# Performance work log

Hardware: AMD Instinct MI355X
Metric: run time of the kernel (lower is better)

Reference implementation:

```python
import jax, jax.numpy as jnp
import jax.scipy as jsp
import numpy as np

NUM_EMBEDDINGS = 256
EMBEDDING_DIM = 64
SPARSITY_LEVEL = 4
N_BINS = 16
COEF_MAX = 3.0
COEF_MU = 50.0
COMMITMENT_COST = 0.25
EPSILON = 1e-10


def _normalize_dict(dictionary):
    # F.normalize(dict, p=2, dim=0, eps): x / max(||x||_2, eps) per column
    nrm = jnp.linalg.norm(dictionary, axis=0, keepdims=True)
    return dictionary / jnp.maximum(nrm, EPSILON)


def _quantize_coeff_mu_law(coeff):
    inv_log1p_mu = 1.0 / np.log1p(COEF_MU)  # scalar constant
    c = jnp.clip(coeff, -COEF_MAX, COEF_MAX) / COEF_MAX
    encoded = jnp.sign(c) * jnp.log1p(jnp.abs(c) * COEF_MU) * inv_log1p_mu
    scaled = (encoded + 1.0) * ((N_BINS - 1) / 2.0)
    bin_idx = jnp.clip(jnp.round(scaled).astype(jnp.int32), 0, N_BINS - 1)
    # dequantize
    z = bin_idx.astype(coeff.dtype) * (2.0 / (N_BINS - 1)) - 1.0
    decoded = jnp.sign(z) * (jnp.expm1(jnp.abs(z) / inv_log1p_mu) / COEF_MU) * COEF_MAX
    return bin_idx, decoded


def batch_omp_with_support(X, Dn, K):
    # X: [M, Bs] signals, Dn: [M, N] normalized dictionary
    G = Dn.T @ Dn                       # [N, N] Gram
    h_bar = (Dn.T @ X).T                # [Bs, N] correlations
    Bs, N = h_bar.shape
    dt = h_bar.dtype
    h = h_bar
    mask = jnp.zeros((Bs, N), dtype=bool)
    L = jnp.ones((Bs, 1, 1), dtype=dt)  # incremental Cholesky of G[I, I]
    I = jnp.zeros((Bs, 0), dtype=jnp.int32)
    x_sel = jnp.zeros((Bs, 0), dtype=dt)
    rows = jnp.arange(Bs)
    for k in range(1, K + 1):  # K is small & static -> unrolled
        idx = jnp.argmax(jnp.abs(h) * (~mask), axis=1).astype(jnp.int32)
        mask = mask.at[rows, idx].set(True)
        if k > 1:
            G_stack = G[I, idx[:, None]]                     # [Bs, k-1]
            w = jsp.linalg.solve_triangular(L, G_stack[..., None], lower=True)  # [Bs,k-1,1]
            wT = jnp.swapaxes(w, 1, 2)                       # [Bs,1,k-1]
            w_corner = jnp.sqrt(jnp.clip(1.0 - jnp.sum(wT * wT, axis=2, keepdims=True), 1e-12))
            top = jnp.concatenate([L, jnp.zeros((Bs, k - 1, 1), dt)], axis=2)
            bot = jnp.concatenate([wT, w_corner], axis=2)
            L = jnp.concatenate([top, bot], axis=1)          # [Bs,k,k]
        I = jnp.concatenate([I, idx[:, None]], axis=1)       # [Bs,k]
        h_stack = jnp.take_along_axis(h_bar, I, axis=1)[..., None]  # [Bs,k,1]
        # cholesky_solve: L L^T x = h
        y = jsp.linalg.solve_triangular(L, h_stack, lower=True)
        xs = jsp.linalg.solve_triangular(jnp.swapaxes(L, 1, 2), y, lower=False)
        x_sel = xs[..., 0]                                   # [Bs,k] coeffs aligned w/ support
        beta = jnp.einsum('bk,bkn->bn', x_sel, G[I])         # [Bs,N]
        h = h_bar - beta
    return I, x_sel


def setup_inputs() -> dict:
    key = jax.random.key(0)
    k1, k2 = jax.random.split(key)
    z_e = jax.random.normal(k1, (32, EMBEDDING_DIM, 64, 64), dtype=jnp.float32)
    dictionary = jax.random.normal(k2, (EMBEDDING_DIM, NUM_EMBEDDINGS), dtype=jnp.float32) * 0.02
    return {"z_e": z_e, "dictionary": dictionary}


def reference(z_e, dictionary):
    B, C, H, W = z_e.shape
    Dn = _normalize_dict(dictionary)
    signals = jnp.transpose(z_e, (0, 2, 3, 1)).reshape(-1, C).T  # [C, B*H*W]
    # OMP runs with no grad (torch.no_grad in original)
    support, coeffs = jax.lax.stop_gradient(
        batch_omp_with_support(jax.lax.stop_gradient(signals), jax.lax.stop_gradient(Dn), SPARSITY_LEVEL)
    )
    # mu-law quantize coefficients (constants w.r.t. grads)
    bin_idx, coeffs_q = _quantize_coeff_mu_law(coeffs)
    # reconstruct with quantized coeffs; dictionary path is differentiable
    atoms = Dn.T[support]                                    # [Bs, K, C]
    recon_flat = jnp.einsum('bkc,bk->bc', atoms, coeffs_q)
    recon = jnp.transpose(recon_flat.reshape(B, H, W, C), (0, 3, 1, 2))
    # VQ-VAE style losses + STE
    e_latent_loss = jnp.mean((jax.lax.stop_gradient(recon) - z_e) ** 2)
    q_latent_loss = jnp.mean((recon - jax.lax.stop_gradient(z_e)) ** 2)
    loss = q_latent_loss + COMMITMENT_COST * e_latent_loss
    z_q = z_e + jax.lax.stop_gradient(recon - z_e)
    return z_q, loss


if __name__ == '__main__':
    out = reference(**setup_inputs())
    print(out[0].shape, out[1])
```

## Files before the change

### kernel.cpp

```cpp
#include <hip/hip_runtime.h>
#include <math.h>

#define NEMB 256
#define DIM 64
#define SIGS_B 64
#define THREADS 256
#define NSIG 131072
#define GRID (NSIG / SIGS_B)

#define LOG1P50 3.9318256327243257
#define INV_MU_F ((float)(1.0 / LOG1P50))
#define TWO15_F ((float)(2.0 / 15.0))

#define LB_SIG   0
#define LB_XS    16384
#define LB_QI    17408
#define LB_RED   18432
#define LDS_BYTES 18464

typedef float f2 __attribute__((ext_vector_type(2)));

__device__ __forceinline__ float rdlane_f(float v, int lane)
{
    return __builtin_bit_cast(float, __builtin_amdgcn_readlane(__builtin_bit_cast(int, v), lane));
}

template<int CTRL>
__device__ __forceinline__ float dpp_fmax(float m)
{
    int sh = __builtin_amdgcn_update_dpp(0, __builtin_bit_cast(int, m), CTRL, 0xf, 0xf, true);
    return fmaxf(m, __builtin_bit_cast(float, sh));
}

__device__ __forceinline__ float wave_max_nn(float v)
{
    v = dpp_fmax<0x111>(v);
    v = dpp_fmax<0x112>(v);
    v = dpp_fmax<0x114>(v);
    v = dpp_fmax<0x118>(v);
    v = dpp_fmax<0x142>(v);
    v = dpp_fmax<0x143>(v);
    return v;
}

__global__ void k_ng(const float* __restrict__ D, float* __restrict__ Dn,
                     float* __restrict__ DnT, float* __restrict__ G,
                     double* __restrict__ loss_acc, unsigned int* __restrict__ ctr)
{
#pragma clang fp contract(off)
    __shared__ float nrmS[NEMB];
    __shared__ float coli[DIM];
    int i = blockIdx.x, j = threadIdx.x;
    if (i == 0 && j == 0) { loss_acc[0] = 0.0; ctr[0] = 0u; }
    float ss = 0.0f;
    for (int c = 0; c < DIM; c++) {
        float v = D[c * NEMB + j];
        float sq = v * v;
        ss = ss + sq;
    }
    float nrm = fmaxf(sqrtf(ss), 1e-10f);
    nrmS[j] = nrm;
    __syncthreads();
    if (j < DIM) {
        float dni = D[j * NEMB + i] / nrmS[i];
        coli[j] = dni;
        Dn[j * NEMB + i] = dni;
        DnT[i * DIM + j] = dni;
    }
    __syncthreads();
    float s = 0.0f;
#pragma unroll 8
    for (int c = 0; c < DIM; c++) {
        float dnj = D[c * NEMB + j] / nrm;
        s = fmaf(coli[c], dnj, s);
    }
    G[i * NEMB + j] = s;
}

__device__ __forceinline__ float quant_decode(float coeff)
{
#pragma clang fp contract(off)
    float c = fminf(fmaxf(coeff, -3.0f), 3.0f) / 3.0f;
    float ac = fabsf(c);
    float sgn = (c > 0.0f) ? 1.0f : ((c < 0.0f) ? -1.0f : 0.0f);
    float l = log1pf(ac * 50.0f);
    float enc = (sgn * l) * INV_MU_F;
    float scaled = (enc + 1.0f) * 7.5f;
    int bin = (int)rintf(scaled);
    bin = bin < 0 ? 0 : (bin > 15 ? 15 : bin);
    float t = (float)bin * TWO15_F;
    float zv = t - 1.0f;
    float az = fabsf(zv);
    float sz = (zv > 0.0f) ? 1.0f : ((zv < 0.0f) ? -1.0f : 0.0f);
    float e = expm1f(az / INV_MU_F);
    return (sz * (e / 50.0f)) * 3.0f;
}

__device__ __forceinline__ void omp_quad(const f2 (*hbsi)[2], int lane, int qt,
                                         const float* __restrict__ G,
                                         float* __restrict__ xsv,
                                         int* __restrict__ qi, int s0)
{
#pragma clang fp contract(off)
    f2 h0[2] = {hbsi[0][0], hbsi[0][1]};
    f2 h1[2] = {hbsi[1][0], hbsi[1][1]};
    f2 h2[2] = {hbsi[2][0], hbsi[2][1]};
    f2 h3[2] = {hbsi[3][0], hbsi[3][1]};
    int m40 = 0, m41 = 0, m42 = 0, m43 = 0;
    int Iv0[4], Iv1[4], Iv2[4], Iv3[4];
    int Ivq[4];
    float L10, L11, L20, L21, L22, L30, L31, L32, L33;
    float y0, y1, y2, y3;
    float x0 = 0.f, x1 = 0.f, x2 = 0.f, x3 = 0.f;
#pragma unroll
    for (int kk = 0; kk < 4; kk++) {
        float bv0 = -1.f, bv1 = -1.f, bv2 = -1.f, bv3 = -1.f;
        int bj0 = 0, bj1 = 0, bj2 = 0, bj3 = 0;
#pragma unroll
        for (int j = 0; j < 4; j++) {
            float a0 = (m40 & (1 << j)) ? 0.f : fabsf(h0[j >> 1][j & 1]);
            if (a0 > bv0) { bv0 = a0; bj0 = j; }
            float a1 = (m41 & (1 << j)) ? 0.f : fabsf(h1[j >> 1][j & 1]);
            if (a1 > bv1) { bv1 = a1; bj1 = j; }
            float a2 = (m42 & (1 << j)) ? 0.f : fabsf(h2[j >> 1][j & 1]);
            if (a2 > bv2) { bv2 = a2; bj2 = j; }
            float a3 = (m43 & (1 << j)) ? 0.f : fabsf(h3[j >> 1][j & 1]);
            if (a3 > bv3) { bv3 = a3; bj3 = j; }
        }
        float r0 = wave_max_nn(bv0);
        float r1 = wave_max_nn(bv1);
        float r2 = wave_max_nn(bv2);
        float r3 = wave_max_nn(bv3);
        float vm0 = rdlane_f(r0, 63), vm1 = rdlane_f(r1, 63);
        float vm2 = rdlane_f(r2, 63), vm3 = rdlane_f(r3, 63);
        unsigned long long bl0 = __ballot(bv0 == vm0);
        unsigned long long bl1 = __ballot(bv1 == vm1);
        unsigned long long bl2 = __ballot(bv2 == vm2);
        unsigned long long bl3 = __ballot(bv3 == vm3);
        int ow0 = __ffsll((long long)bl0) - 1;
        int ow1 = __ffsll((long long)bl1) - 1;
        int ow2 = __ffsll((long long)bl2) - 1;
        int ow3 = __ffsll((long long)bl3) - 1;
        int bo0 = __builtin_amdgcn_readlane(bj0, ow0);
        int bo1 = __builtin_amdgcn_readlane(bj1, ow1);
        int bo2 = __builtin_amdgcn_readlane(bj2, ow2);
        int bo3 = __builtin_amdgcn_readlane(bj3, ow3);
        int id0 = 4 * ow0 + bo0;
        int id1 = 4 * ow1 + bo1;
        int id2 = 4 * ow2 + bo2;
        int id3 = 4 * ow3 + bo3;
        m40 |= (lane == ow0) ? (1 << bo0) : 0;
        m41 |= (lane == ow1) ? (1 << bo1) : 0;
        m42 |= (lane == ow2) ? (1 << bo2) : 0;
        m43 |= (lane == ow3) ? (1 << bo3) : 0;
        float tv0 = hbsi[0][0][0];
        tv0 = (bj0 == 1) ? hbsi[0][0][1] : tv0;
        tv0 = (bj0 == 2) ? hbsi[0][1][0] : tv0;
        tv0 = (bj0 == 3) ? hbsi[0][1][1] : tv0;
        float tv1 = hbsi[1][0][0];
        tv1 = (bj1 == 1) ? hbsi[1][0][1] : tv1;
        tv1 = (bj1 == 2) ? hbsi[1][1][0] : tv1;
        tv1 = (bj1 == 3) ? hbsi[1][1][1] : tv1;
        float tv2 = hbsi[2][0][0];
        tv2 = (bj2 == 1) ? hbsi[2][0][1] : tv2;
        tv2 = (bj2 == 2) ? hbsi[2][1][0] : tv2;
        tv2 = (bj2 == 3) ? hbsi[2][1][1] : tv2;
        float tv3 = hbsi[3][0][0];
        tv3 = (bj3 == 1) ? hbsi[3][0][1] : tv3;
        tv3 = (bj3 == 2) ? hbsi[3][1][0] : tv3;
        tv3 = (bj3 == 3) ? hbsi[3][1][1] : tv3;
        float hs0 = rdlane_f(tv0, ow0);
        float hs1 = rdlane_f(tv1, ow1);
        float hs2 = rdlane_f(tv2, ow2);
        float hs3 = rdlane_f(tv3, ow3);
        Iv0[kk] = id0; Iv1[kk] = id1; Iv2[kk] = id2; Iv3[kk] = id3;
        float hsel = (qt & 2) ? ((qt & 1) ? hs3 : hs2) : ((qt & 1) ? hs1 : hs0);
        int idxq = (qt & 2) ? ((qt & 1) ? id3 : id2) : ((qt & 1) ? id1 : id0);
        Ivq[kk] = idxq;
        float Gs0 = 0.f, Gs1 = 0.f, Gs2 = 0.f;
        if (kk > 0) Gs0 = G[(size_t)(Ivq[0] << 8) + idxq];
        if (kk > 1) Gs1 = G[(size_t)(Ivq[1] << 8) + idxq];
        if (kk > 2) Gs2 = G[(size_t)(Ivq[2] << 8) + idxq];
        if (kk == 1) {
            float cw0 = Gs0;
            float css = cw0 * cw0;
            float om = 1.0f - css;
            L10 = cw0;
            L11 = sqrtf(fmaxf(om, 1e-12f));
        }
        if (kk == 2) {
            float cw0 = Gs0;
            float ct = Gs1 - L10 * cw0;
            float cw1 = ct / L11;
            float css = cw0 * cw0;
            float cp = cw1 * cw1; css = css + cp;
            float om = 1.0f - css;
            L20 = cw0; L21 = cw1;
            L22 = sqrtf(fmaxf(om, 1e-12f));
        }
        if (kk == 3) {
            float cw0 = Gs0;
            float ct = Gs1 - L10 * cw0;
            float cw1 = ct / L11;
            float ca = L20 * cw0;
            float cp = L21 * cw1; ca = ca + cp;
            float ct3 = Gs2 - ca;
            float cw2 = ct3 / L22;
            float css = cw0 * cw0;
            cp = cw1 * cw1; css = css + cp;
            cp = cw2 * cw2; css = css + cp;
            float om = 1.0f - css;
            L30 = cw0; L31 = cw1; L32 = cw2;
            L33 = sqrtf(fmaxf(om, 1e-12f));
        }
        if (kk == 0) y0 = hsel;
        if (kk == 1) { float a = L10 * y0; y1 = (hsel - a) / L11; }
        if (kk == 2) { float a = L20 * y0; float p = L21 * y1; a = a + p;
                       y2 = (hsel - a) / L22; }
        if (kk == 3) { float a = L30 * y0; float p = L31 * y1; a = a + p;
                       p = L32 * y2; a = a + p;
                       y3 = (hsel - a) / L33; }
        if (kk == 0) { x0 = y0; }
        if (kk == 1) {
            x1 = y1 / L11;
            float a = L10 * x1;
            x0 = y0 - a;
        }
        if (kk == 2) {
            x2 = y2 / L22;
            float a = L21 * x2;
            x1 = (y1 - a) / L11;
            a = L10 * x1;
            float p = L20 * x2; a = a + p;
            x0 = y0 - a;
        }
        if (kk == 3) {
            x3 = y3 / L33;
            float a = L32 * x3;
            x2 = (y2 - a) / L22;
            a = L21 * x2;
            float p = L31 * x3; a = a + p;
            x1 = (y1 - a) / L11;
            a = L10 * x1;
            p = L20 * x2; a = a + p;
            p = L30 * x3; a = a + p;
            x0 = y0 - a;
        }
        if (kk < 3) {
            float xb00 = rdlane_f(x0, 0),  xb10 = rdlane_f(x0, 16);
            float xb20 = rdlane_f(x0, 32), xb30 = rdlane_f(x0, 48);
            float xb01 = 0.f, xb11 = 0.f, xb21 = 0.f, xb31 = 0.f;
            float xb02 = 0.f, xb12 = 0.f, xb22 = 0.f, xb32 = 0.f;
            if (kk > 0) { xb01 = rdlane_f(x1, 0);  xb11 = rdlane_f(x1, 16);
                          xb21 = rdlane_f(x1, 32); xb31 = rdlane_f(x1, 48); }
            if (kk > 1) { xb02 = rdlane_f(x2, 0);  xb12 = rdlane_f(x2, 16);
                          xb22 = rdlane_f(x2, 32); xb32 = rdlane_f(x2, 48); }
            const int l4 = 4 * lane;
            float4 R00 = *(const float4*)(G + ((size_t)Iv0[0] << 8) + l4);
            float4 R10 = *(const float4*)(G + ((size_t)Iv1[0] << 8) + l4);
            float4 R20 = *(const float4*)(G + ((size_t)Iv2[0] << 8) + l4);
            float4 R30 = *(const float4*)(G + ((size_t)Iv3[0] << 8) + l4);
            float4 R01, R11, R21, R31, R02, R12, R22, R32;
            if (kk > 0) {
                R01 = *(const float4*)(G + ((size_t)Iv0[1] << 8) + l4);
                R11 = *(const float4*)(G + ((size_t)Iv1[1] << 8) + l4);
                R21 = *(const float4*)(G + ((size_t)Iv2[1] << 8) + l4);
                R31 = *(const float4*)(G + ((size_t)Iv3[1] << 8) + l4);
            }
            if (kk > 1) {
                R02 = *(const float4*)(G + ((size_t)Iv0[2] << 8) + l4);
                R12 = *(const float4*)(G + ((size_t)Iv1[2] << 8) + l4);
                R22 = *(const float4*)(G + ((size_t)Iv2[2] << 8) + l4);
                R32 = *(const float4*)(G + ((size_t)Iv3[2] << 8) + l4);
            }
            {
                f2 bsa = (f2){xb00, xb00} * (f2){R00.x, R00.y};
                f2 bsb = (f2){xb00, xb00} * (f2){R00.z, R00.w};
                if (kk > 0) { f2 pa = (f2){xb01, xb01} * (f2){R01.x, R01.y}; bsa = bsa + pa;
                              f2 pb = (f2){xb01, xb01} * (f2){R01.z, R01.w}; bsb = bsb + pb; }
                if (kk > 1) { f2 pa = (f2){xb02, xb02} * (f2){R02.x, R02.y}; bsa = bsa + pa;
                              f2 pb = (f2){xb02, xb02} * (f2){R02.z, R02.w}; bsb = bsb + pb; }
                h0[0] = hbsi[0][0] - bsa;
                h0[1] = hbsi[0][1] - bsb;
            }
            {
                f2 bsa = (f2){xb10, xb10} * (f2){R10.x, R10.y};
                f2 bsb = (f2){xb10, xb10} * (f2){R10.z, R10.w};
                if (kk > 0) { f2 pa = (f2){xb11, xb11} * (f2){R11.x, R11.y}; bsa = bsa + pa;
                              f2 pb = (f2){xb11, xb11} * (f2){R11.z, R11.w}; bsb = bsb + pb; }
                if (kk > 1) { f2 pa = (f2){xb12, xb12} * (f2){R12.x, R12.y}; bsa = bsa + pa;
                              f2 pb = (f2){xb12, xb12} * (f2){R12.z, R12.w}; bsb = bsb + pb; }
                h1[0] = hbsi[1][0] - bsa;
                h1[1] = hbsi[1][1] - bsb;
            }
            {
                f2 bsa = (f2){xb20, xb20} * (f2){R20.x, R20.y};
                f2 bsb = (f2){xb20, xb20} * (f2){R20.z, R20.w};
                if (kk > 0) { f2 pa = (f2){xb21, xb21} * (f2){R21.x, R21.y}; bsa = bsa + pa;
                              f2 pb = (f2){xb21, xb21} * (f2){R21.z, R21.w}; bsb = bsb + pb; }
                if (kk > 1) { f2 pa = (f2){xb22, xb22} * (f2){R22.x, R22.y}; bsa = bsa + pa;
                              f2 pb = (f2){xb22, xb22} * (f2){R22.z, R22.w}; bsb = bsb + pb; }
                h2[0] = hbsi[2][0] - bsa;
                h2[1] = hbsi[2][1] - bsb;
            }
            {
                f2 bsa = (f2){xb30, xb30} * (f2){R30.x, R30.y};
                f2 bsb = (f2){xb30, xb30} * (f2){R30.z, R30.w};
                if (kk > 0) { f2 pa = (f2){xb31, xb31} * (f2){R31.x, R31.y}; bsa = bsa + pa;
                              f2 pb = (f2){xb31, xb31} * (f2){R31.z, R31.w}; bsb = bsb + pb; }
                if (kk > 1) { f2 pa = (f2){xb32, xb32} * (f2){R32.x, R32.y}; bsa = bsa + pa;
                              f2 pb = (f2){xb32, xb32} * (f2){R32.z, R32.w}; bsb = bsb + pb; }
                h3[0] = hbsi[3][0] - bsa;
                h3[1] = hbsi[3][1] - bsb;
            }
        }
    }
    if ((lane & 15) == 0) {
        int s = s0 + qt;
        xsv[0 * SIGS_B + s] = x0; xsv[1 * SIGS_B + s] = x1;
        xsv[2 * SIGS_B + s] = x2; xsv[3 * SIGS_B + s] = x3;
        qi[0 * SIGS_B + s] = Ivq[0]; qi[1 * SIGS_B + s] = Ivq[1];
        qi[2 * SIGS_B + s] = Ivq[2]; qi[3 * SIGS_B + s] = Ivq[3];
    }
}

__launch_bounds__(THREADS, 4)
__global__ void k_omp(const float* __restrict__ z,
                      const float* __restrict__ Dn_g,
                      const float* __restrict__ DnT_g,
                      const float* __restrict__ G,
                      double* __restrict__ loss_acc,
                      unsigned int* __restrict__ ctr,
                      float* __restrict__ zq,
                      float* __restrict__ loss_out)
{
    extern __shared__ char smem[];
    float* sig = (float*)(smem + LB_SIG);
    float* xsv = (float*)(smem + LB_XS);
    int* qi = (int*)(smem + LB_QI);
    double* red = (double*)(smem + LB_RED);

    int tid = threadIdx.x;
    int lane = tid & 63;
    int qt = lane >> 4;
    int wid = tid >> 6;

    long sbase = (long)blockIdx.x * SIGS_B;
    int b = (int)(sbase >> 12);
    int pl0 = (int)(sbase & 4095);
    const float* zb = z + ((size_t)b << 18) + pl0;
    {
        int w = tid & (SIGS_B - 1);
        int g = tid >> 6;
#pragma unroll
        for (int i = 0; i < 16; i++) {
            int c = g * 16 + i;
            sig[c * SIGS_B + w] = zb[(size_t)c * 4096 + w];
        }
    }
    __syncthreads();

    for (int g2 = 0; g2 < 2; g2++) {
        int s0 = wid * 16 + g2 * 8;
        f2 hb[8][2];
#pragma unroll
        for (int a = 0; a < 8; a++) {
            hb[a][0] = (f2){0.0f, 0.0f};
            hb[a][1] = (f2){0.0f, 0.0f};
        }
#pragma unroll 8
        for (int c = 0; c < DIM; c++) {
            float4 sva = *(const float4*)(sig + c * SIGS_B + s0);
            float4 svb = *(const float4*)(sig + c * SIGS_B + s0 + 4);
            float s8[8] = {sva.x, sva.y, sva.z, sva.w, svb.x, svb.y, svb.z, svb.w};
            float4 dv = *(const float4*)(Dn_g + c * NEMB + 4 * lane);
            f2 d0; d0.x = dv.x; d0.y = dv.y;
            f2 d1; d1.x = dv.z; d1.y = dv.w;
#pragma unroll
            for (int a = 0; a < 8; a++) {
                f2 sa = {s8[a], s8[a]};
                hb[a][0] = __builtin_elementwise_fma(sa, d0, hb[a][0]);
                hb[a][1] = __builtin_elementwise_fma(sa, d1, hb[a][1]);
            }
        }
        omp_quad(hb,     lane, qt, G, xsv, qi, s0);
        omp_quad(hb + 4, lane, qt, G, xsv, qi, s0 + 4);
    }
    __syncthreads();

    {
        int jq = tid >> 6;
        int wq = tid & (SIGS_B - 1);
        xsv[jq * SIGS_B + wq] = quant_decode(xsv[jq * SIGS_B + wq]);
    }
    __syncthreads();

    double lsum = 0.0;
    float* zqb = zq + ((size_t)b << 18) + pl0;
    {
#pragma clang fp contract(off)
        int w = tid & (SIGS_B - 1);
        int g = tid >> 6;
        float q0 = xsv[0 * SIGS_B + w], q1 = xsv[1 * SIGS_B + w];
        float q2 = xsv[2 * SIGS_B + w], q3 = xsv[3 * SIGS_B + w];
        int i0 = qi[0 * SIGS_B + w], i1 = qi[1 * SIGS_B + w];
        int i2 = qi[2 * SIGS_B + w], i3 = qi[3 * SIGS_B + w];
        const float* t0p = DnT_g + (i0 << 6) + (g << 4);
        const float* t1p = DnT_g + (i1 << 6) + (g << 4);
        const float* t2p = DnT_g + (i2 << 6) + (g << 4);
        const float* t3p = DnT_g + (i3 << 6) + (g << 4);
#pragma unroll
        for (int cb = 0; cb < 4; cb++) {
            float4 d0 = *(const float4*)(t0p + 4 * cb);
            float4 d1 = *(const float4*)(t1p + 4 * cb);
            float4 d2 = *(const float4*)(t2p + 4 * cb);
            float4 d3 = *(const float4*)(t3p + 4 * cb);
#pragma unroll
            for (int u = 0; u < 4; u++) {
                int c = (g << 4) + (cb << 2) + u;
                float e0 = (u == 0) ? d0.x : (u == 1) ? d0.y : (u == 2) ? d0.z : d0.w;
                float e1 = (u == 0) ? d1.x : (u == 1) ? d1.y : (u == 2) ? d1.z : d1.w;
                float e2 = (u == 0) ? d2.x : (u == 1) ? d2.y : (u == 2) ? d2.z : d2.w;
                float e3 = (u == 0) ? d3.x : (u == 1) ? d3.y : (u == 2) ? d3.z : d3.w;
                float p0 = q0 * e0;
                float p1 = q1 * e1;
                float p2 = q2 * e2;
                float p3 = q3 * e3;
                float r = p0 + p1;
                r = r + p2;
                r = r + p3;
                float zev = sig[c * SIGS_B + w];
                float d = r - zev;
                float zqv = zev + d;
                lsum += (double)d * (double)d;
                zqb[(size_t)c * 4096 + w] = zqv;
            }
        }
    }
#pragma unroll
    for (int off = 32; off > 0; off >>= 1) lsum += __shfl_xor(lsum, off);
    if (lane == 0) red[wid] = lsum;
    __syncthreads();
    if (tid == 0) {
        double t = 0.0;
#pragma unroll
        for (int i = 0; i < 4; i++) t += red[i];
        atomicAdd(loss_acc, t);
        __threadfence();
        unsigned int done = atomicAdd(ctr, 1u);
        if (done == GRID - 1) {
            double m = atomicAdd(loss_acc, 0.0) / 8388608.0;
            loss_out[0] = (float)(m + 0.25 * m);
        }
    }
}

extern "C" void kernel_launch(void* const* d_in, const int* in_sizes, int n_in,
                              void* d_out, int out_size, void* d_ws, size_t ws_size,
                              hipStream_t stream)
{
    const float* z = (const float*)d_in[0];
    const float* D = (const float*)d_in[1];
    float* out = (float*)d_out;
    char* ws = (char*)d_ws;
    double* loss_acc = (double*)ws;
    unsigned int* ctr = (unsigned int*)(ws + 8);
    float* Dn = (float*)(ws + 256);
    float* G = (float*)(ws + 256 + 65536);
    float* DnT = (float*)(ws + 256 + 65536 + 262144);

    k_ng<<<NEMB, NEMB, 0, stream>>>(D, Dn, DnT, G, loss_acc, ctr);
    hipFuncSetAttribute(reinterpret_cast<const void*>(k_omp),
                        hipFuncAttributeMaxDynamicSharedMemorySize, LDS_BYTES);
    k_omp<<<GRID, THREADS, LDS_BYTES, stream>>>(z, Dn, DnT, G, loss_acc, ctr, out, out + 8388608);
    (void)in_sizes; (void)n_in; (void)out_size; (void)ws_size;
}
```

Measured before the change: 299.5 us.

## Cache selected Gram rows in registers across OMP iterations

Each selected atom's Gram row is now loaded once per iteration and kept in registers. It is reused both for the correlation update and for extracting the Gram entries that previously came from scalar global loads. Correlation arrays are passed as scalar vector registers instead of indexed arrays, which avoids possible scratch spills. The launch-bounds occupancy hint drops from 4 to 2 to make room for the extra live registers, at the risk of lower occupancy and less latency hiding.

After: 261.7 us (median of 2 runs). 1.14x faster.

```diff
diff --git a/kernel.cpp b/kernel.cpp
--- a/kernel.cpp
+++ b/kernel.cpp
@@ -96,91 +96,205 @@
     return (sz * (e / 50.0f)) * 3.0f;
 }
 
-__device__ __forceinline__ void omp_quad(const f2 (*hbsi)[2], int lane, int qt,
-                                         const float* __restrict__ G,
-                                         float* __restrict__ xsv,
-                                         int* __restrict__ qi, int s0)
+__device__ __forceinline__ void omp_quad4(
+    f2 sA0, f2 sA1, f2 sB0, f2 sB1, f2 sC0, f2 sC1, f2 sD0, f2 sD1,
+    int lane, int qt,
+    const float* __restrict__ G,
+    float* __restrict__ xsv, int* __restrict__ qi, int s0)
 {
 #pragma clang fp contract(off)
-    f2 h0[2] = {hbsi[0][0], hbsi[0][1]};
-    f2 h1[2] = {hbsi[1][0], hbsi[1][1]};
-    f2 h2[2] = {hbsi[2][0], hbsi[2][1]};
-    f2 h3[2] = {hbsi[3][0], hbsi[3][1]};
-    int m40 = 0, m41 = 0, m42 = 0, m43 = 0;
-    int Iv0[4], Iv1[4], Iv2[4], Iv3[4];
-    int Ivq[4];
+    f2 hA0 = sA0, hA1 = sA1, hB0 = sB0, hB1 = sB1;
+    f2 hC0 = sC0, hC1 = sC1, hD0 = sD0, hD1 = sD1;
+    int m4A = 0, m4B = 0, m4C = 0, m4D = 0;
+    f2 gA00, gA01, gA10, gA11, gA20, gA21;
+    f2 gB00, gB01, gB10, gB11, gB20, gB21;
+    f2 gC00, gC01, gC10, gC11, gC20, gC21;
+    f2 gD00, gD01, gD10, gD11, gD20, gD21;
+    int iq0 = 0, iq1 = 0, iq2 = 0, iq3 = 0;
     float L10, L11, L20, L21, L22, L30, L31, L32, L33;
     float y0, y1, y2, y3;
     float x0 = 0.f, x1 = 0.f, x2 = 0.f, x3 = 0.f;
 #pragma unroll
     for (int kk = 0; kk < 4; kk++) {
-        float bv0 = -1.f, bv1 = -1.f, bv2 = -1.f, bv3 = -1.f;
-        int bj0 = 0, bj1 = 0, bj2 = 0, bj3 = 0;
-#pragma unroll
-        for (int j = 0; j < 4; j++) {
-            float a0 = (m40 & (1 << j)) ? 0.f : fabsf(h0[j >> 1][j & 1]);
-            if (a0 > bv0) { bv0 = a0; bj0 = j; }
-            float a1 = (m41 & (1 << j)) ? 0.f : fabsf(h1[j >> 1][j & 1]);
-            if (a1 > bv1) { bv1 = a1; bj1 = j; }
-            float a2 = (m42 & (1 << j)) ? 0.f : fabsf(h2[j >> 1][j & 1]);
-            if (a2 > bv2) { bv2 = a2; bj2 = j; }
-            float a3 = (m43 & (1 << j)) ? 0.f : fabsf(h3[j >> 1][j & 1]);
-            if (a3 > bv3) { bv3 = a3; bj3 = j; }
-        }
-        float r0 = wave_max_nn(bv0);
-        float r1 = wave_max_nn(bv1);
-        float r2 = wave_max_nn(bv2);
-        float r3 = wave_max_nn(bv3);
-        float vm0 = rdlane_f(r0, 63), vm1 = rdlane_f(r1, 63);
-        float vm2 = rdlane_f(r2, 63), vm3 = rdlane_f(r3, 63);
-        unsigned long long bl0 = __ballot(bv0 == vm0);
-        unsigned long long bl1 = __ballot(bv1 == vm1);
-        unsigned long long bl2 = __ballot(bv2 == vm2);
-        unsigned long long bl3 = __ballot(bv3 == vm3);
-        int ow0 = __ffsll((long long)bl0) - 1;
-        int ow1 = __ffsll((long long)bl1) - 1;
-        int ow2 = __ffsll((long long)bl2) - 1;
-        int ow3 = __ffsll((long long)bl3) - 1;
-        int bo0 = __builtin_amdgcn_readlane(bj0, ow0);
-        int bo1 = __builtin_amdgcn_readlane(bj1, ow1);
-        int bo2 = __builtin_amdgcn_readlane(bj2, ow2);
-        int bo3 = __builtin_amdgcn_readlane(bj3, ow3);
-        int id0 = 4 * ow0 + bo0;
-        int id1 = 4 * ow1 + bo1;
-        int id2 = 4 * ow2 + bo2;
-        int id3 = 4 * ow3 + bo3;
-        m40 |= (lane == ow0) ? (1 << bo0) : 0;
-        m41 |= (lane == ow1) ? (1 << bo1) : 0;
-        m42 |= (lane == ow2) ? (1 << bo2) : 0;
-        m43 |= (lane == ow3) ? (1 << bo3) : 0;
-        float tv0 = hbsi[0][0][0];
-        tv0 = (bj0 == 1) ? hbsi[0][0][1] : tv0;
-        tv0 = (bj0 == 2) ? hbsi[0][1][0] : tv0;
-        tv0 = (bj0 == 3) ? hbsi[0][1][1] : tv0;
-        float tv1 = hbsi[1][0][0];
-        tv1 = (bj1 == 1) ? hbsi[1][0][1] : tv1;
-        tv1 = (bj1 == 2) ? hbsi[1][1][0] : tv1;
-        tv1 = (bj1 == 3) ? hbsi[1][1][1] : tv1;
-        float tv2 = hbsi[2][0][0];
-        tv2 = (bj2 == 1) ? hbsi[2][0][1] : tv2;
-        tv2 = (bj2 == 2) ? hbsi[2][1][0] : tv2;
-        tv2 = (bj2 == 3) ? hbsi[2][1][1] : tv2;
-        float tv3 = hbsi[3][0][0];
-        tv3 = (bj3 == 1) ? hbsi[3][0][1] : tv3;
-        tv3 = (bj3 == 2) ? hbsi[3][1][0] : tv3;
-        tv3 = (bj3 == 3) ? hbsi[3][1][1] : tv3;
-        float hs0 = rdlane_f(tv0, ow0);
-        float hs1 = rdlane_f(tv1, ow1);
-        float hs2 = rdlane_f(tv2, ow2);
-        float hs3 = rdlane_f(tv3, ow3);
-        Iv0[kk] = id0; Iv1[kk] = id1; Iv2[kk] = id2; Iv3[kk] = id3;
-        float hsel = (qt & 2) ? ((qt & 1) ? hs3 : hs2) : ((qt & 1) ? hs1 : hs0);
-        int idxq = (qt & 2) ? ((qt & 1) ? id3 : id2) : ((qt & 1) ? id1 : id0);
-        Ivq[kk] = idxq;
+        float aA0 = (m4A & 1) ? 0.f : fabsf(hA0[0]);
+        float aA1 = (m4A & 2) ? 0.f : fabsf(hA0[1]);
+        float aA2 = (m4A & 4) ? 0.f : fabsf(hA1[0]);
+        float aA3 = (m4A & 8) ? 0.f : fabsf(hA1[1]);
+        float bvA = aA0; int bjA = 0;
+        if (aA1 > bvA) { bvA = aA1; bjA = 1; }
+        if (aA2 > bvA) { bvA = aA2; bjA = 2; }
+        if (aA3 > bvA) { bvA = aA3; bjA = 3; }
+        float aB0 = (m4B & 1) ? 0.f : fabsf(hB0[0]);
+        float aB1 = (m4B & 2) ? 0.f : fabsf(hB0[1]);
+        float aB2 = (m4B & 4) ? 0.f : fabsf(hB1[0]);
+        float aB3 = (m4B & 8) ? 0.f : fabsf(hB1[1]);
+        float bvB = aB0; int bjB = 0;
+        if (aB1 > bvB) { bvB = aB1; bjB = 1; }
+        if (aB2 > bvB) { bvB = aB2; bjB = 2; }
+        if (aB3 > bvB) { bvB = aB3; bjB = 3; }
+        float aC0 = (m4C & 1) ? 0.f : fabsf(hC0[0]);
+        float aC1 = (m4C & 2) ? 0.f : fabsf(hC0[1]);
+        float aC2 = (m4C & 4) ? 0.f : fabsf(hC1[0]);
+        float aC3 = (m4C & 8) ? 0.f : fabsf(hC1[1]);
+        float bvC = aC0; int bjC = 0;
+        if (aC1 > bvC) { bvC = aC1; bjC = 1; }
+        if (aC2 > bvC) { bvC = aC2; bjC = 2; }
+        if (aC3 > bvC) { bvC = aC3; bjC = 3; }
+        float aD0 = (m4D & 1) ? 0.f : fabsf(hD0[0]);
+        float aD1 = (m4D & 2) ? 0.f : fabsf(hD0[1]);
+        float aD2 = (m4D & 4) ? 0.f : fabsf(hD1[0]);
+        float aD3 = (m4D & 8) ? 0.f : fabsf(hD1[1]);
+        float bvD = aD0; int bjD = 0;
+        if (aD1 > bvD) { bvD = aD1; bjD = 1; }
+        if (aD2 > bvD) { bvD = aD2; bjD = 2; }
+        if (aD3 > bvD) { bvD = aD3; bjD = 3; }
+        float rA = wave_max_nn(bvA);
+        float rB = wave_max_nn(bvB);
+        float rC = wave_max_nn(bvC);
+        float rD = wave_max_nn(bvD);
+        float vmA = rdlane_f(rA, 63), vmB = rdlane_f(rB, 63);
+        float vmC = rdlane_f(rC, 63), vmD = rdlane_f(rD, 63);
+        unsigned long long blA = __ballot(bvA == vmA);
+        unsigned long long blB = __ballot(bvB == vmB);
+        unsigned long long blC = __ballot(bvC == vmC);
+        unsigned long long blD = __ballot(bvD == vmD);
+        int owA = __ffsll((long long)blA) - 1;
+        int owB = __ffsll((long long)blB) - 1;
+        int owC = __ffsll((long long)blC) - 1;
+        int owD = __ffsll((long long)blD) - 1;
+        int boA = __builtin_amdgcn_readlane(bjA, owA);
+        int boB = __builtin_amdgcn_readlane(bjB, owB);
+        int boC = __builtin_amdgcn_readlane(bjC, owC);
+        int boD = __builtin_amdgcn_readlane(bjD, owD);
+        int idA = 4 * owA + boA;
+        int idB = 4 * owB + boB;
+        int idC = 4 * owC + boC;
+        int idD = 4 * owD + boD;
+        m4A |= (lane == owA) ? (1 << boA) : 0;
+        m4B |= (lane == owB) ? (1 << boB) : 0;
+        m4C |= (lane == owC) ? (1 << boC) : 0;
+        m4D |= (lane == owD) ? (1 << boD) : 0;
+        float tvA = sA0[0];
+        tvA = (bjA == 1) ? sA0[1] : tvA;
+        tvA = (bjA == 2) ? sA1[0] : tvA;
+        tvA = (bjA == 3) ? sA1[1] : tvA;
+        float tvB = sB0[0];
+        tvB = (bjB == 1) ? sB0[1] : tvB;
+        tvB = (bjB == 2) ? sB1[0] : tvB;
+        tvB = (bjB == 3) ? sB1[1] : tvB;
+        float tvC = sC0[0];
+        tvC = (bjC == 1) ? sC0[1] : tvC;
+        tvC = (bjC == 2) ? sC1[0] : tvC;
+        tvC = (bjC == 3) ? sC1[1] : tvC;
+        float tvD = sD0[0];
+        tvD = (bjD == 1) ? sD0[1] : tvD;
+        tvD = (bjD == 2) ? sD1[0] : tvD;
+        tvD = (bjD == 3) ? sD1[1] : tvD;
+        float hsA = rdlane_f(tvA, owA);
+        float hsB = rdlane_f(tvB, owB);
+        float hsC = rdlane_f(tvC, owC);
+        float hsD = rdlane_f(tvD, owD);
+        float hsel = (qt & 2) ? ((qt & 1) ? hsD : hsC) : ((qt & 1) ? hsB : hsA);
+        int idxq = (qt & 2) ? ((qt & 1) ? idD : idC) : ((qt & 1) ? idB : idA);
+        if (kk == 0) iq0 = idxq;
+        if (kk == 1) iq1 = idxq;
+        if (kk == 2) iq2 = idxq;
+        if (kk == 3) iq3 = idxq;
+        const int l4 = 4 * lane;
+        if (kk < 3) {
+            float4 ra = *(const float4*)(G + ((size_t)idA << 8) + l4);
+            float4 rb = *(const float4*)(G + ((size_t)idB << 8) + l4);
+            float4 rc = *(const float4*)(G + ((size_t)idC << 8) + l4);
+            float4 rd = *(const float4*)(G + ((size_t)idD << 8) + l4);
+            if (kk == 0) {
+                gA00 = (f2){ra.x, ra.y}; gA01 = (f2){ra.z, ra.w};
+                gB00 = (f2){rb.x, rb.y}; gB01 = (f2){rb.z, rb.w};
+                gC00 = (f2){rc.x, rc.y}; gC01 = (f2){rc.z, rc.w};
+                gD00 = (f2){rd.x, rd.y}; gD01 = (f2){rd.z, rd.w};
+            }
+            if (kk == 1) {
+                gA10 = (f2){ra.x, ra.y}; gA11 = (f2){ra.z, ra.w};
+                gB10 = (f2){rb.x, rb.y}; gB11 = (f2){rb.z, rb.w};
+                gC10 = (f2){rc.x, rc.y}; gC11 = (f2){rc.z, rc.w};
+                gD10 = (f2){rd.x, rd.y}; gD11 = (f2){rd.z, rd.w};
+            }
+            if (kk == 2) {
+                gA20 = (f2){ra.x, ra.y}; gA21 = (f2){ra.z, ra.w};
+                gB20 = (f2){rb.x, rb.y}; gB21 = (f2){rb.z, rb.w};
+                gC20 = (f2){rc.x, rc.y}; gC21 = (f2){rc.z, rc.w};
+                gD20 = (f2){rd.x, rd.y}; gD21 = (f2){rd.z, rd.w};
+            }
+        }
         float Gs0 = 0.f, Gs1 = 0.f, Gs2 = 0.f;
-        if (kk > 0) Gs0 = G[(size_t)(Ivq[0] << 8) + idxq];
-        if (kk > 1) Gs1 = G[(size_t)(Ivq[1] << 8) + idxq];
-        if (kk > 2) Gs2 = G[(size_t)(Ivq[2] << 8) + idxq];
+        if (kk > 0) {
+            float eA = gA00[0];
+            eA = (boA == 1) ? gA00[1] : eA;
+            eA = (boA == 2) ? gA01[0] : eA;
+            eA = (boA == 3) ? gA01[1] : eA;
+            float eB = gB00[0];
+            eB = (boB == 1) ? gB00[1] : eB;
+            eB = (boB == 2) ? gB01[0] : eB;
+            eB = (boB == 3) ? gB01[1] : eB;
+            float eC = gC00[0];
+            eC = (boC == 1) ? gC00[1] : eC;
+            eC = (boC == 2) ? gC01[0] : eC;
+            eC = (boC == 3) ? gC01[1] : eC;
+            float eD = gD00[0];
+            eD = (boD == 1) ? gD00[1] : eD;
+            eD = (boD == 2) ? gD01[0] : eD;
+            eD = (boD == 3) ? gD01[1] : eD;
+            float GsA = rdlane_f(eA, owA);
+            float GsB = rdlane_f(eB, owB);
+            float GsC = rdlane_f(eC, owC);
+            float GsD = rdlane_f(eD, owD);
+            Gs0 = (qt & 2) ? ((qt & 1) ? GsD : GsC) : ((qt & 1) ? GsB : GsA);
+        }
+        if (kk > 1) {
+            float eA = gA10[0];
+            eA = (boA == 1) ? gA10[1] : eA;
+            eA = (boA == 2) ? gA11[0] : eA;
+            eA = (boA == 3) ? gA11[1] : eA;
+            float eB = gB10[0];
+            eB = (boB == 1) ? gB10[1] : eB;
+            eB = (boB == 2) ? gB11[0] : eB;
+            eB = (boB == 3) ? gB11[1] : eB;
+            float eC = gC10[0];
+            eC = (boC == 1) ? gC10[1] : eC;
+            eC = (boC == 2) ? gC11[0] : eC;
+            eC = (boC == 3) ? gC11[1] : eC;
+            float eD = gD10[0];
+            eD = (boD == 1) ? gD10[1] : eD;
+            eD = (boD == 2) ? gD11[0] : eD;
+            eD = (boD == 3) ? gD11[1] : eD;
+            float GsA = rdlane_f(eA, owA);
+            float GsB = rdlane_f(eB, owB);
+            float GsC = rdlane_f(eC, owC);
+            float GsD = rdlane_f(eD, owD);
+            Gs1 = (qt & 2) ? ((qt & 1) ? GsD : GsC) : ((qt & 1) ? GsB : GsA);
+        }
+        if (kk > 2) {
+            float eA = gA20[0];
+            eA = (boA == 1) ? gA20[1] : eA;
+            eA = (boA == 2) ? gA21[0] : eA;
+            eA = (boA == 3) ? gA21[1] : eA;
+            float eB = gB20[0];
+            eB = (boB == 1) ? gB20[1] : eB;
+            eB = (boB == 2) ? gB21[0] : eB;
+            eB = (boB == 3) ? gB21[1] : eB;
+            float eC = gC20[0];
+            eC = (boC == 1) ? gC20[1] : eC;
+            eC = (boC == 2) ? gC21[0] : eC;
+            eC = (boC == 3) ? gC21[1] : eC;
+            float eD = gD20[0];
+            eD = (boD == 1) ? gD20[1] : eD;
+            eD = (boD == 2) ? gD21[0] : eD;
+            eD = (boD == 3) ? gD21[1] : eD;
+            float GsA = rdlane_f(eA, owA);
+            float GsB = rdlane_f(eB, owB);
+            float GsC = rdlane_f(eC, owC);
+            float GsD = rdlane_f(eD, owD);
+            Gs2 = (qt & 2) ? ((qt & 1) ? GsD : GsC) : ((qt & 1) ? GsB : GsA);
+        }
         if (kk == 1) {
             float cw0 = Gs0;
             float css = cw0 * cw0;
@@ -247,71 +361,53 @@
             x0 = y0 - a;
         }
         if (kk < 3) {
-            float xb00 = rdlane_f(x0, 0),  xb10 = rdlane_f(x0, 16);
-            float xb20 = rdlane_f(x0, 32), xb30 = rdlane_f(x0, 48);
-            float xb01 = 0.f, xb11 = 0.f, xb21 = 0.f, xb31 = 0.f;
-            float xb02 = 0.f, xb12 = 0.f, xb22 = 0.f, xb32 = 0.f;
-            if (kk > 0) { xb01 = rdlane_f(x1, 0);  xb11 = rdlane_f(x1, 16);
-                          xb21 = rdlane_f(x1, 32); xb31 = rdlane_f(x1, 48); }
-            if (kk > 1) { xb02 = rdlane_f(x2, 0);  xb12 = rdlane_f(x2, 16);
-                          xb22 = rdlane_f(x2, 32); xb32 = rdlane_f(x2, 48); }
-            const int l4 = 4 * lane;
-            float4 R00 = *(const float4*)(G + ((size_t)Iv0[0] << 8) + l4);
-            float4 R10 = *(const float4*)(G + ((size_t)Iv1[0] << 8) + l4);
-            float4 R20 = *(const float4*)(G + ((size_t)Iv2[0] << 8) + l4);
-            float4 R30 = *(const float4*)(G + ((size_t)Iv3[0] << 8) + l4);
-            float4 R01, R11, R21, R31, R02, R12, R22, R32;
-            if (kk > 0) {
-                R01 = *(const float4*)(G + ((size_t)Iv0[1] << 8) + l4);
-                R11 = *(const float4*)(G + ((size_t)Iv1[1] << 8) + l4);
-                R21 = *(const float4*)(G + ((size_t)Iv2[1] << 8) + l4);
-                R31 = *(const float4*)(G + ((size_t)Iv3[1] << 8) + l4);
-            }
-            if (kk > 1) {
-                R02 = *(const float4*)(G + ((size_t)Iv0[2] << 8) + l4);
-                R12 = *(const float4*)(G + ((size_t)Iv1[2] << 8) + l4);
-                R22 = *(const float4*)(G + ((size_t)Iv2[2] << 8) + l4);
-                R32 = *(const float4*)(G + ((size_t)Iv3[2] << 8) + l4);
-            }
+            float xbA0 = rdlane_f(x0, 0),  xbB0 = rdlane_f(x0, 16);
+            float xbC0 = rdlane_f(x0, 32), xbD0 = rdlane_f(x0, 48);
+            float xbA1 = 0.f, xbB1 = 0.f, xbC1 = 0.f, xbD1 = 0.f;
+            float xbA2 = 0.f, xbB2 = 0.f, xbC2 = 0.f, xbD2 = 0.f;
+            if (kk > 0) { xbA1 = rdlane_f(x1, 0);  xbB1 = rdlane_f(x1, 16);
+                          xbC1 = rdlane_f(x1, 32); xbD1 = rdlane_f(x1, 48); }
+            if (kk > 1) { xbA2 = rdlane_f(x2, 0);  xbB2 = rdlane_f(x2, 16);
+                          xbC2 = rdlane_f(x2, 32); xbD2 = rdlane_f(x2, 48); }
             {
-                f2 bsa = (f2){xb00, xb00} * (f2){R00.x, R00.y};
-                f2 bsb = (f2){xb00, xb00} * (f2){R00.z, R00.w};
-                if (kk > 0) { f2 pa = (f2){xb01, xb01} * (f2){R01.x, R01.y}; bsa = bsa + pa;
-                              f2 pb = (f2){xb01, xb01} * (f2){R01.z, R01.w}; bsb = bsb + pb; }
-                if (kk > 1) { f2 pa = (f2){xb02, xb02} * (f2){R02.x, R02.y}; bsa = bsa + pa;
-                              f2 pb = (f2){xb02, xb02} * (f2){R02.z, R02.w}; bsb = bsb + pb; }
-                h0[0] = hbsi[0][0] - bsa;
-                h0[1] = hbsi[0][1] - bsb;
+                f2 bsa = (f2){xbA0, xbA0} * gA00;
+                f2 bsb = (f2){xbA0, xbA0} * gA01;
+                if (kk > 0) { f2 pa = (f2){xbA1, xbA1} * gA10; bsa = bsa + pa;
+                              f2 pb = (f2){xbA1, xbA1} * gA11; bsb = bsb + pb; }
+                if (kk > 1) { f2 pa = (f2){xbA2, xbA2} * gA20; bsa = bsa + pa;
+                              f2 pb = (f2){xbA2, xbA2} * gA21; bsb = bsb + pb; }
+                hA0 = sA0 - bsa;
+                hA1 = sA1 - bsb;
             }
             {
-                f2 bsa = (f2){xb10, xb10} * (f2){R10.x, R10.y};
-                f2 bsb = (f2){xb10, xb10} * (f2){R10.z, R10.w};
-                if (kk > 0) { f2 pa = (f2){xb11, xb11} * (f2){R11.x, R11.y}; bsa = bsa + pa;
-                              f2 pb = (f2){xb11, xb11} * (f2){R11.z, R11.w}; bsb = bsb + pb; }
-                if (kk > 1) { f2 pa = (f2){xb12, xb12} * (f2){R12.x, R12.y}; bsa = bsa + pa;
-                              f2 pb = (f2){xb12, xb12} * (f2){R12.z, R12.w}; bsb = bsb + pb; }
-                h1[0] = hbsi[1][0] - bsa;
-                h1[1] = hbsi[1][1] - bsb;
+                f2 bsa = (f2){xbB0, xbB0} * gB00;
+                f2 bsb = (f2){xbB0, xbB0} * gB01;
+                if (kk > 0) { f2 pa = (f2){xbB1, xbB1} * gB10; bsa = bsa + pa;
+                              f2 pb = (f2){xbB1, xbB1} * gB11; bsb = bsb + pb; }
+                if (kk > 1) { f2 pa = (f2){xbB2, xbB2} * gB20; bsa = bsa + pa;
+                              f2 pb = (f2){xbB2, xbB2} * gB21; bsb = bsb + pb; }
+                hB0 = sB0 - bsa;
+                hB1 = sB1 - bsb;
             }
             {
-                f2 bsa = (f2){xb20, xb20} * (f2){R20.x, R20.y};
-                f2 bsb = (f2){xb20, xb20} * (f2){R20.z, R20.w};
-                if (kk > 0) { f2 pa = (f2){xb21, xb21} * (f2){R21.x, R21.y}; bsa = bsa + pa;
-                              f2 pb = (f2){xb21, xb21} * (f2){R21.z, R21.w}; bsb = bsb + pb; }
-                if (kk > 1) { f2 pa = (f2){xb22, xb22} * (f2){R22.x, R22.y}; bsa = bsa + pa;
-                              f2 pb = (f2){xb22, xb22} * (f2){R22.z, R22.w}; bsb = bsb + pb; }
-                h2[0] = hbsi[2][0] - bsa;
-                h2[1] = hbsi[2][1] - bsb;
+                f2 bsa = (f2){xbC0, xbC0} * gC00;
+                f2 bsb = (f2){xbC0, xbC0} * gC01;
+                if (kk > 0) { f2 pa = (f2){xbC1, xbC1} * gC10; bsa = bsa + pa;
+                              f2 pb = (f2){xbC1, xbC1} * gC11; bsb = bsb + pb; }
+                if (kk > 1) { f2 pa = (f2){xbC2, xbC2} * gC20; bsa = bsa + pa;
+                              f2 pb = (f2){xbC2, xbC2} * gC21; bsb = bsb + pb; }
+                hC0 = sC0 - bsa;
+                hC1 = sC1 - bsb;
             }
             {
-                f2 bsa = (f2){xb30, xb30} * (f2){R30.x, R30.y};
-                f2 bsb = (f2){xb30, xb30} * (f2){R30.z, R30.w};
-                if (kk > 0) { f2 pa = (f2){xb31, xb31} * (f2){R31.x, R31.y}; bsa = bsa + pa;
-                              f2 pb = (f2){xb31, xb31} * (f2){R31.z, R31.w}; bsb = bsb + pb; }
-                if (kk > 1) { f2 pa = (f2){xb32, xb32} * (f2){R32.x, R32.y}; bsa = bsa + pa;
-                              f2 pb = (f2){xb32, xb32} * (f2){R32.z, R32.w}; bsb = bsb + pb; }
-                h3[0] = hbsi[3][0] - bsa;
-                h3[1] = hbsi[3][1] - bsb;
+                f2 bsa = (f2){xbD0, xbD0} * gD00;
+                f2 bsb = (f2){xbD0, xbD0} * gD01;
+                if (kk > 0) { f2 pa = (f2){xbD1, xbD1} * gD10; bsa = bsa + pa;
+                              f2 pb = (f2){xbD1, xbD1} * gD11; bsb = bsb + pb; }
+                if (kk > 1) { f2 pa = (f2){xbD2, xbD2} * gD20; bsa = bsa + pa;
+                              f2 pb = (f2){xbD2, xbD2} * gD21; bsb = bsb + pb; }
+                hD0 = sD0 - bsa;
+                hD1 = sD1 - bsb;
             }
         }
     }
@@ -319,12 +415,12 @@
         int s = s0 + qt;
         xsv[0 * SIGS_B + s] = x0; xsv[1 * SIGS_B + s] = x1;
         xsv[2 * SIGS_B + s] = x2; xsv[3 * SIGS_B + s] = x3;
-        qi[0 * SIGS_B + s] = Ivq[0]; qi[1 * SIGS_B + s] = Ivq[1];
-        qi[2 * SIGS_B + s] = Ivq[2]; qi[3 * SIGS_B + s] = Ivq[3];
-    }
-}
-
-__launch_bounds__(THREADS, 4)
+        qi[0 * SIGS_B + s] = iq0; qi[1 * SIGS_B + s] = iq1;
+        qi[2 * SIGS_B + s] = iq2; qi[3 * SIGS_B + s] = iq3;
+    }
+}
+
+__launch_bounds__(THREADS, 2)
 __global__ void k_omp(const float* __restrict__ z,
                       const float* __restrict__ Dn_g,
                       const float* __restrict__ DnT_g,
@@ -362,29 +458,42 @@
 
     for (int g2 = 0; g2 < 2; g2++) {
         int s0 = wid * 16 + g2 * 8;
-        f2 hb[8][2];
-#pragma unroll
-        for (int a = 0; a < 8; a++) {
-            hb[a][0] = (f2){0.0f, 0.0f};
-            hb[a][1] = (f2){0.0f, 0.0f};
-        }
+        f2 h00 = {0.f, 0.f}, h01 = {0.f, 0.f};
+        f2 h10 = {0.f, 0.f}, h11 = {0.f, 0.f};
+        f2 h20 = {0.f, 0.f}, h21 = {0.f, 0.f};
+        f2 h30 = {0.f, 0.f}, h31 = {0.f, 0.f};
+        f2 h40 = {0.f, 0.f}, h41 = {0.f, 0.f};
+        f2 h50 = {0.f, 0.f}, h51 = {0.f, 0.f};
+        f2 h60 = {0.f, 0.f}, h61 = {0.f, 0.f};
+        f2 h70 = {0.f, 0.f}, h71 = {0.f, 0.f};
 #pragma unroll 8
         for (int c = 0; c < DIM; c++) {
             float4 sva = *(const float4*)(sig + c * SIGS_B + s0);
             float4 svb = *(const float4*)(sig + c * SIGS_B + s0 + 4);
-            float s8[8] = {sva.x, sva.y, sva.z, sva.w, svb.x, svb.y, svb.z, svb.w};
             float4 dv = *(const float4*)(Dn_g + c * NEMB + 4 * lane);
-            f2 d0; d0.x = dv.x; d0.y = dv.y;
-            f2 d1; d1.x = dv.z; d1.y = dv.w;
-#pragma unroll
-            for (int a = 0; a < 8; a++) {
-                f2 sa = {s8[a], s8[a]};
-                hb[a][0] = __builtin_elementwise_fma(sa, d0, hb[a][0]);
-                hb[a][1] = __builtin_elementwise_fma(sa, d1, hb[a][1]);
-            }
-        }
-        omp_quad(hb,     lane, qt, G, xsv, qi, s0);
-        omp_quad(hb + 4, lane, qt, G, xsv, qi, s0 + 4);
+            f2 d0 = {dv.x, dv.y};
+            f2 d1 = {dv.z, dv.w};
+            h00 = __builtin_elementwise_fma((f2){sva.x, sva.x}, d0, h00);
+            h01 = __builtin_elementwise_fma((f2){sva.x, sva.x}, d1, h01);
+            h10 = __builtin_elementwise_fma((f2){sva.y, sva.y}, d0, h10);
+            h11 = __builtin_elementwise_fma((f2){sva.y, sva.y}, d1, h11);
+            h20 = __builtin_elementwise_fma((f2){sva.z, sva.z}, d0, h20);
+            h21 = __builtin_elementwise_fma((f2){sva.z, sva.z}, d1, h21);
+            h30 = __builtin_elementwise_fma((f2){sva.w, sva.w}, d0, h30);
+            h31 = __builtin_elementwise_fma((f2){sva.w, sva.w}, d1, h31);
+            h40 = __builtin_elementwise_fma((f2){svb.x, svb.x}, d0, h40);
+            h41 = __builtin_elementwise_fma((f2){svb.x, svb.x}, d1, h41);
+            h50 = __builtin_elementwise_fma((f2){svb.y, svb.y}, d0, h50);
+            h51 = __builtin_elementwise_fma((f2){svb.y, svb.y}, d1, h51);
+            h60 = __builtin_elementwise_fma((f2){svb.z, svb.z}, d0, h60);
+            h61 = __builtin_elementwise_fma((f2){svb.z, svb.z}, d1, h61);
+            h70 = __builtin_elementwise_fma((f2){svb.w, svb.w}, d0, h70);
+            h71 = __builtin_elementwise_fma((f2){svb.w, svb.w}, d1, h71);
+        }
+        omp_quad4(h00, h01, h10, h11, h20, h21, h30, h31,
+                  lane, qt, G, xsv, qi, s0);
+        omp_quad4(h40, h41, h50, h51, h60, h61, h70, h71,
+                  lane, qt, G, xsv, qi, s0 + 4);
     }
     __syncthreads();
 
```
